# Kernel tuning notes

Hardware: AMD Instinct MI355X
Metric: run time of the kernel (lower is better)

Reference implementation:

```python
import jax, jax.numpy as jnp
import numpy as np

T, B, DIM = 1024, 32, 1024
H, N = 8, 64
INIT_BETA_BIAS = 2.0
EPS = 1e-6


def setup_inputs() -> dict:
    key = jax.random.key(0)
    ks = jax.random.split(key, 5)
    scale = 1.0 / np.sqrt(DIM)  # xavier-ish
    return {
        "x": jax.random.normal(ks[0], (T, B, DIM), dtype=jnp.float32),
        "W_k": jax.random.normal(ks[1], (H * N, DIM), dtype=jnp.float32) * scale,
        "W_v": jax.random.normal(ks[2], (H * N, DIM), dtype=jnp.float32) * scale,
        "W_q": jax.random.normal(ks[3], (H * N, DIM), dtype=jnp.float32) * scale,
        "W_beta": jax.random.normal(ks[4], (H * N, DIM), dtype=jnp.float32) * scale,
        "b_beta": jnp.full((H, N), INIT_BETA_BIAS, dtype=jnp.float32),
    }


def reference(x, W_k, W_v, W_q, W_beta, b_beta):
    Tn, Bn, D = x.shape
    Hn, n = b_beta.shape
    xf = x.reshape(Tn * Bn, D)
    k_all = (xf @ W_k.T).reshape(Tn, Bn, Hn, n)
    v_all = (xf @ W_v.T).reshape(Tn, Bn, Hn, n)
    q_all = (xf @ W_q.T).reshape(Tn, Bn, Hn, n)
    beta_all = jax.nn.sigmoid((xf @ W_beta.T).reshape(Tn, Bn, Hn, n) + b_beta)
    k_norm = k_all / (jnp.linalg.norm(k_all, axis=-1, keepdims=True) + EPS)

    def step(S, inp):
        k, v, q, beta = inp  # each [B, H, n]
        retrieved = jnp.einsum('bhij,bhj->bhi', S, k)
        delta = v - retrieved
        outer = jnp.einsum('bhi,bhj->bhij', delta, k)
        S = jnp.tanh(beta[..., None] * S + outer)
        Sq = jnp.einsum('bhij,bhj->bhi', S, q)
        out = Sq * jax.nn.silu(Sq)  # [B, H, n]
        return S, out.reshape(Bn, Hn * n)

    S0 = jnp.zeros((Bn, Hn, n, n), dtype=x.dtype)
    S_final, output = jax.lax.scan(step, S0, (k_norm, v_all, q_all, beta_all))
    return output, S_final  # output: [T, B, H*n]
```

## Files before the change

### kernel.cpp

```cpp
#include <hip/hip_runtime.h>
#include <stdint.h>

#define TSTEPS 1024
#define BATCH  32
#define DIMK   1024
#define HEADS  8
#define NHEAD  64
#define NPROJ  2048
#define MROWS  (TSTEPS*BATCH)

typedef _Float16 f16;
typedef _Float16 f16x2 __attribute__((ext_vector_type(2)));
typedef _Float16 f16x4 __attribute__((ext_vector_type(4)));
typedef _Float16 f16x8 __attribute__((ext_vector_type(8)));
typedef float    f32x2 __attribute__((ext_vector_type(2)));
typedef float    f32x4 __attribute__((ext_vector_type(4)));
typedef unsigned int u32;

#define AS_GLOBAL __attribute__((address_space(1)))
#define AS_LDS    __attribute__((address_space(3)))

#define C2LOG2E 2.8853900817779268f

__device__ __forceinline__ void load_lds_16B(const void* g, void* l){
  __builtin_amdgcn_global_load_lds((const AS_GLOBAL u32*)g, (AS_LDS u32*)l, 16, 0, 0);
}

__device__ __forceinline__ float sigmoid_fast(float x){
  return __builtin_amdgcn_rcpf(1.0f + __expf(-x));
}

__device__ __forceinline__ float exp2_fast(float x){
#if __has_builtin(__builtin_amdgcn_exp2f)
  return __builtin_amdgcn_exp2f(x);
#else
  return __expf(0.6931471805599453f * x);
#endif
}

__device__ __forceinline__ float fdot2(f16x2 a, f16x2 b, float c){
#if __has_builtin(__builtin_amdgcn_fdot2)
  typedef __fp16 h16x2 __attribute__((ext_vector_type(2)));
  return __builtin_amdgcn_fdot2(__builtin_bit_cast(h16x2, a),
                                __builtin_bit_cast(h16x2, b), c, false);
#else
  return fmaf((float)a[1], (float)b[1], fmaf((float)a[0], (float)b[0], c));
#endif
}

__device__ __forceinline__ f16x2 pack2(float a, float b){
#if __has_builtin(__builtin_amdgcn_cvt_pkrtz)
  return __builtin_bit_cast(f16x2, __builtin_amdgcn_cvt_pkrtz(a, b));
#else
  f16x2 r = { (f16)a, (f16)b };
  return r;
#endif
}

template<int CTRL>
__device__ __forceinline__ float dpp_add(float r){
  int x = __builtin_amdgcn_update_dpp(__builtin_bit_cast(int, r),
                                      __builtin_bit_cast(int, r),
                                      CTRL, 0xf, 0xf, false);
  return r + __builtin_bit_cast(float, x);
}
__device__ __forceinline__ float dpp_reduce16(float r){
  r = dpp_add<0x121>(r);
  r = dpp_add<0x122>(r);
  r = dpp_add<0x124>(r);
  r = dpp_add<0x128>(r);
  return r;
}

__global__ __launch_bounds__(256) void cast_kernel(const float4* __restrict__ src,
                                                   f16x4* __restrict__ dst, int n4){
  int i = blockIdx.x*blockDim.x + threadIdx.x;
  int stride = gridDim.x*blockDim.x;
  for (; i < n4; i += stride){
    float4 v = src[i];
    f16x4 o = { (f16)v.x, (f16)v.y, (f16)v.z, (f16)v.w };
    dst[i] = o;
  }
}

#define BM 128
#define BN 128
#define BK 32

__global__ __launch_bounds__(256) void gemm_xwT(const f16* __restrict__ A,
                                                const f16* __restrict__ B,
                                                f16* __restrict__ C){
  __shared__ f16 sA[BM*BK];
  __shared__ f16 sB[BN*BK];
  const int t = threadIdx.x;
  const int w = t >> 6;
  const int l = t & 63;
  const int bm = blockIdx.x;
  const int bn = blockIdx.y;
  const int wr = w >> 1, wc = w & 1;

  f32x4 acc[4][4] = {};

  const int srow = t >> 2;
  const int scol = (t & 3) * 8;
  const f16* gA0 = A + (size_t)(bm*BM + srow)*DIMK + scol;
  const f16* gB0 = B + (size_t)(bn*BN + srow)*DIMK + scol;
  char* sAb = (char*)sA;
  char* sBb = (char*)sB;
  const int ldsw = w*1024;

  for (int kk = 0; kk < DIMK/BK; ++kk){
    const f16* pa = gA0 + kk*BK;
    const f16* pb = gB0 + kk*BK;
    load_lds_16B(pa,           sAb + ldsw);
    load_lds_16B(pa + 64*DIMK, sAb + ldsw + 4096);
    load_lds_16B(pb,           sBb + ldsw);
    load_lds_16B(pb + 64*DIMK, sBb + ldsw + 4096);
    __syncthreads();

    f16x8 af[4], bf[4];
    #pragma unroll
    for (int mi=0; mi<4; ++mi){
      int arow = wr*64 + mi*16 + (l & 15);
      af[mi] = *(const f16x8*)(sAb + arow*64 + (l>>4)*16);
    }
    #pragma unroll
    for (int ni=0; ni<4; ++ni){
      int brow = wc*64 + ni*16 + (l & 15);
      bf[ni] = *(const f16x8*)(sBb + brow*64 + (l>>4)*16);
    }
    #pragma unroll
    for (int mi=0; mi<4; ++mi)
      #pragma unroll
      for (int ni=0; ni<4; ++ni)
        acc[mi][ni] = __builtin_amdgcn_mfma_f32_16x16x32_f16(af[mi], bf[ni], acc[mi][ni], 0, 0, 0);
    __syncthreads();
  }

  const int crow0 = bm*BM + wr*64 + (l>>4)*4;
  const int ccol0 = bn*BN + wc*64 + (l & 15);
  #pragma unroll
  for (int mi=0; mi<4; ++mi)
    #pragma unroll
    for (int ni=0; ni<4; ++ni)
      #pragma unroll
      for (int r=0; r<4; ++r)
        C[(size_t)(crow0 + mi*16 + r)*NPROJ + ccol0 + ni*16] = (f16)acc[mi][ni][r];
}

__global__ __launch_bounds__(256) void prep_kernel(f16* __restrict__ Y,
                                                   const float* __restrict__ b_beta){
  int g = blockIdx.x*4 + (threadIdx.x >> 6);
  int l = threadIdx.x & 63;
  int h = g & 7;
  f16* y = Y + (size_t)(g >> 3)*NPROJ + h*NHEAD + l;
  float k  = (float)y[0];
  float br = (float)y[1536];
  float ss = k*k;
  #pragma unroll
  for (int d=1; d<64; d<<=1) ss += __shfl_xor(ss, d);
  y[0]    = (f16)(k * __builtin_amdgcn_rcpf(__builtin_sqrtf(ss) + 1e-6f));
  y[1536] = (f16)(C2LOG2E * sigmoid_fast(br + b_beta[h*NHEAD + l]));
}

struct Stage { f16x2 kl, kh, ql, qh; float v, bb; };

__device__ __forceinline__ Stage load_stage(const f16* base, int tn, int cb, int row){
  const f16* pn = base + (size_t)tn * (BATCH*NPROJ);
  Stage s;
  uint2 ku = *(const uint2*)(pn + cb);
  uint2 qu = *(const uint2*)(pn + 1024 + cb);
  s.kl = __builtin_bit_cast(f16x2, ku.x);
  s.kh = __builtin_bit_cast(f16x2, ku.y);
  s.ql = __builtin_bit_cast(f16x2, qu.x);
  s.qh = __builtin_bit_cast(f16x2, qu.y);
  s.v  = (float)pn[512 + row];
  s.bb = (float)pn[1536 + row];
  return s;
}

__device__ __forceinline__ void step_compute(const Stage& st, int tt, int g,
                                             f32x2& S01, f32x2& S23,
                                             f16x2& P0, f16x2& P1,
                                             float* outp){
  float r = fdot2(P1, st.kh, fdot2(P0, st.kl, 0.f));
  r = dpp_reduce16(r);
  float dl = (st.v - r) * C2LOG2E;

  f32x2 d2  = { dl, dl };
  f32x2 bb2 = { st.bb, st.bb };
  f32x2 k01 = { (float)st.kl[0], (float)st.kl[1] };
  f32x2 k23 = { (float)st.kh[0], (float)st.kh[1] };
  f32x2 arg01 = bb2*S01 + d2*k01;
  f32x2 arg23 = bb2*S23 + d2*k23;

  f32x2 e01 = { exp2_fast(arg01.x), exp2_fast(arg01.y) };
  f32x2 e23 = { exp2_fast(arg23.x), exp2_fast(arg23.y) };
  f32x2 one2 = { 1.f, 1.f };
  e01 += one2;  e23 += one2;
  f32x2 t01 = { __builtin_amdgcn_rcpf(e01.x), __builtin_amdgcn_rcpf(e01.y) };
  f32x2 t23 = { __builtin_amdgcn_rcpf(e23.x), __builtin_amdgcn_rcpf(e23.y) };
  f32x2 m2 = { -2.f, -2.f };
  S01 = m2*t01 + one2;
  S23 = m2*t23 + one2;
  P0 = pack2(S01.x, S01.y);
  P1 = pack2(S23.x, S23.y);

  float sq = fdot2(P1, st.qh, fdot2(P0, st.ql, 0.f));
  sq = dpp_reduce16(sq);
  if (g == 0) outp[(size_t)tt * (BATCH*512)] = sq;
}

__global__ __launch_bounds__(1024) void scan_kernel(const f16* __restrict__ Y,
                                                    float* __restrict__ out,
                                                    float* __restrict__ S_out){
  const int p = blockIdx.x;
  const int b = p >> 3, h = p & 7;
  const int t = threadIdx.x;
  const int row = t >> 4;
  const int g   = t & 15;
  const int cb  = g*4;

  f32x2 S01 = {0.f, 0.f}, S23 = {0.f, 0.f};
  f16x2 P0 = {}, P1 = {};

  const f16* base = Y + (size_t)b*NPROJ + h*NHEAD;
  float* outp = out + (size_t)b*512 + h*NHEAD + row;

  Stage s0 = load_stage(base, 0, cb, row);
  Stage s1 = load_stage(base, 1, cb, row);
  Stage s2 = load_stage(base, 2, cb, row);
  Stage s3 = load_stage(base, 3, cb, row);

  #pragma unroll 1
  for (int tt=0; tt<TSTEPS; tt+=4){
    Stage n0 = load_stage(base, tt+4, cb, row);
    step_compute(s0, tt,   g, S01,S23, P0,P1, outp);
    Stage n1 = load_stage(base, tt+5, cb, row);
    step_compute(s1, tt+1, g, S01,S23, P0,P1, outp);
    Stage n2 = load_stage(base, tt+6, cb, row);
    step_compute(s2, tt+2, g, S01,S23, P0,P1, outp);
    Stage n3 = load_stage(base, tt+7, cb, row);
    step_compute(s3, tt+3, g, S01,S23, P0,P1, outp);
    s0 = n0; s1 = n1; s2 = n2; s3 = n3;
  }

  size_t sbase = ((size_t)p*NHEAD + row)*NHEAD + cb;
  float4 v4 = { S01.x, S01.y, S23.x, S23.y };
  *(float4*)(S_out + sbase) = v4;
}

__global__ __launch_bounds__(256) void silu_kernel(float4* __restrict__ o, int n4){
  int i = blockIdx.x*blockDim.x + threadIdx.x;
  int stride = gridDim.x*blockDim.x;
  for (; i < n4; i += stride){
    float4 v = o[i];
    v.x = v.x*v.x*sigmoid_fast(v.x);
    v.y = v.y*v.y*sigmoid_fast(v.y);
    v.z = v.z*v.z*sigmoid_fast(v.z);
    v.w = v.w*v.w*sigmoid_fast(v.w);
    o[i] = v;
  }
}

extern "C" void kernel_launch(void* const* d_in, const int* in_sizes, int n_in,
                              void* d_out, int out_size, void* d_ws, size_t ws_size,
                              hipStream_t stream){
  const float* x  = (const float*)d_in[0];
  const float* Wk = (const float*)d_in[1];
  const float* Wv = (const float*)d_in[2];
  const float* Wq = (const float*)d_in[3];
  const float* Wb = (const float*)d_in[4];
  const float* bb = (const float*)d_in[5];

  float* out = (float*)d_out;
  float* Sf  = out + (size_t)TSTEPS*BATCH*512;

  char* ws = (char*)d_ws;
  f16* Yh = (f16*)ws;
  f16* xh = (f16*)(ws + 134217728);
  f16* wh = (f16*)(ws + 134217728 + 67108864);

  cast_kernel<<<2048, 256, 0, stream>>>((const float4*)x,  (f16x4*)xh, (MROWS*DIMK)/4);
  cast_kernel<<<512,  256, 0, stream>>>((const float4*)Wk, (f16x4*)(wh + 0*524288), 524288/4);
  cast_kernel<<<512,  256, 0, stream>>>((const float4*)Wv, (f16x4*)(wh + 1*524288), 524288/4);
  cast_kernel<<<512,  256, 0, stream>>>((const float4*)Wq, (f16x4*)(wh + 2*524288), 524288/4);
  cast_kernel<<<512,  256, 0, stream>>>((const float4*)Wb, (f16x4*)(wh + 3*524288), 524288/4);

  dim3 g(MROWS/BM, NPROJ/BN);
  gemm_xwT<<<g, 256, 0, stream>>>(xh, wh, Yh);

  prep_kernel<<<(TSTEPS*BATCH*HEADS)/4, 256, 0, stream>>>(Yh, bb);

  scan_kernel<<<256, 1024, 0, stream>>>(Yh, out, Sf);

  silu_kernel<<<2048, 256, 0, stream>>>((float4*)out, (TSTEPS*BATCH*512)/4);
}
```

Measured before the change: 802.5 us.

## Store projections per (batch,head) contiguously and stream scan inputs via LDS double buffer

The GEMM epilogue now writes its output in a [b,h,t,256] layout, with k, q and interleaved v/beta per step, in place of row-major [t*b, 2048]. Each scan block can then read its whole time series contiguously. The scan kernel copies 64-step chunks into a double-buffered LDS region with async global-to-LDS loads, replacing per-step scattered global loads, and the prep kernel is adapted to the new layout. The aim is to take global load latency off the serial recurrence. The cost is scattered 2-byte stores in the GEMM epilogue and a block-wide barrier every 64 steps.

```diff
diff --git a/kernel.cpp b/kernel.cpp
--- a/kernel.cpp
+++ b/kernel.cpp
@@ -89,7 +89,7 @@
 
 __global__ __launch_bounds__(256) void gemm_xwT(const f16* __restrict__ A,
                                                 const f16* __restrict__ B,
-                                                f16* __restrict__ C){
+                                                f16* __restrict__ Zo){
   __shared__ f16 sA[BM*BK];
   __shared__ f16 sB[BN*BK];
   const int t = threadIdx.x;
@@ -140,112 +140,124 @@
   const int crow0 = bm*BM + wr*64 + (l>>4)*4;
   const int ccol0 = bn*BN + wc*64 + (l & 15);
   #pragma unroll
-  for (int mi=0; mi<4; ++mi)
+  for (int ni=0; ni<4; ++ni){
+    int n = ccol0 + ni*16;
+    int stream = n >> 9;
+    int hh = (n >> 6) & 7;
+    int e = n & 63;
+    int eidx = (stream==0) ? e : (stream==2) ? 64+e : (stream==1) ? 128+2*e : 129+2*e;
     #pragma unroll
-    for (int ni=0; ni<4; ++ni)
+    for (int mi=0; mi<4; ++mi)
       #pragma unroll
-      for (int r=0; r<4; ++r)
-        C[(size_t)(crow0 + mi*16 + r)*NPROJ + ccol0 + ni*16] = (f16)acc[mi][ni][r];
-}
-
-__global__ __launch_bounds__(256) void prep_kernel(f16* __restrict__ Y,
+      for (int r=0; r<4; ++r){
+        int m = crow0 + mi*16 + r;
+        int ti = m >> 5, bi = m & 31;
+        size_t zi = ((size_t)(bi*8 + hh)*1024 + ti)*256 + eidx;
+        Zo[zi] = (f16)acc[mi][ni][r];
+      }
+  }
+}
+
+__global__ __launch_bounds__(256) void prep_kernel(f16* __restrict__ Z,
                                                    const float* __restrict__ b_beta){
-  int g = blockIdx.x*4 + (threadIdx.x >> 6);
+  int wid = blockIdx.x*4 + (threadIdx.x >> 6);
   int l = threadIdx.x & 63;
-  int h = g & 7;
-  f16* y = Y + (size_t)(g >> 3)*NPROJ + h*NHEAD + l;
-  float k  = (float)y[0];
-  float br = (float)y[1536];
+  int h = (wid >> 10) & 7;
+  f16* z = Z + (size_t)wid * 256;
+  float k  = (float)z[l];
+  float br = (float)z[129 + 2*l];
   float ss = k*k;
   #pragma unroll
   for (int d=1; d<64; d<<=1) ss += __shfl_xor(ss, d);
-  y[0]    = (f16)(k * __builtin_amdgcn_rcpf(__builtin_sqrtf(ss) + 1e-6f));
-  y[1536] = (f16)(C2LOG2E * sigmoid_fast(br + b_beta[h*NHEAD + l]));
-}
-
-struct Stage { f16x2 kl, kh, ql, qh; float v, bb; };
-
-__device__ __forceinline__ Stage load_stage(const f16* base, int tn, int cb, int row){
-  const f16* pn = base + (size_t)tn * (BATCH*NPROJ);
-  Stage s;
-  uint2 ku = *(const uint2*)(pn + cb);
-  uint2 qu = *(const uint2*)(pn + 1024 + cb);
-  s.kl = __builtin_bit_cast(f16x2, ku.x);
-  s.kh = __builtin_bit_cast(f16x2, ku.y);
-  s.ql = __builtin_bit_cast(f16x2, qu.x);
-  s.qh = __builtin_bit_cast(f16x2, qu.y);
-  s.v  = (float)pn[512 + row];
-  s.bb = (float)pn[1536 + row];
-  return s;
-}
-
-__device__ __forceinline__ void step_compute(const Stage& st, int tt, int g,
-                                             f32x2& S01, f32x2& S23,
-                                             f16x2& P0, f16x2& P1,
-                                             float* outp){
-  float r = fdot2(P1, st.kh, fdot2(P0, st.kl, 0.f));
-  r = dpp_reduce16(r);
-  float dl = (st.v - r) * C2LOG2E;
-
-  f32x2 d2  = { dl, dl };
-  f32x2 bb2 = { st.bb, st.bb };
-  f32x2 k01 = { (float)st.kl[0], (float)st.kl[1] };
-  f32x2 k23 = { (float)st.kh[0], (float)st.kh[1] };
-  f32x2 arg01 = bb2*S01 + d2*k01;
-  f32x2 arg23 = bb2*S23 + d2*k23;
-
-  f32x2 e01 = { exp2_fast(arg01.x), exp2_fast(arg01.y) };
-  f32x2 e23 = { exp2_fast(arg23.x), exp2_fast(arg23.y) };
-  f32x2 one2 = { 1.f, 1.f };
-  e01 += one2;  e23 += one2;
-  f32x2 t01 = { __builtin_amdgcn_rcpf(e01.x), __builtin_amdgcn_rcpf(e01.y) };
-  f32x2 t23 = { __builtin_amdgcn_rcpf(e23.x), __builtin_amdgcn_rcpf(e23.y) };
-  f32x2 m2 = { -2.f, -2.f };
-  S01 = m2*t01 + one2;
-  S23 = m2*t23 + one2;
-  P0 = pack2(S01.x, S01.y);
-  P1 = pack2(S23.x, S23.y);
-
-  float sq = fdot2(P1, st.qh, fdot2(P0, st.ql, 0.f));
-  sq = dpp_reduce16(sq);
-  if (g == 0) outp[(size_t)tt * (BATCH*512)] = sq;
-}
-
-__global__ __launch_bounds__(1024) void scan_kernel(const f16* __restrict__ Y,
+  z[l]       = (f16)(k * __builtin_amdgcn_rcpf(__builtin_sqrtf(ss) + 1e-6f));
+  z[129+2*l] = (f16)(C2LOG2E * sigmoid_fast(br + b_beta[h*NHEAD + l]));
+}
+
+#define STAGE_STEPS 64
+#define STAGE_F16   (STAGE_STEPS*256)
+
+__global__ __launch_bounds__(1024) void scan_kernel(const f16* __restrict__ Z,
                                                     float* __restrict__ out,
                                                     float* __restrict__ S_out){
   const int p = blockIdx.x;
   const int b = p >> 3, h = p & 7;
   const int t = threadIdx.x;
+  const int w = t >> 6;
+  const int lane = t & 63;
   const int row = t >> 4;
   const int g   = t & 15;
-  const int cb  = g*4;
-
-  f32x2 S01 = {0.f, 0.f}, S23 = {0.f, 0.f};
+
+  __shared__ f16 lds[2*STAGE_F16];
+
+  f32x2 S01 = {0.f,0.f}, S23 = {0.f,0.f};
   f16x2 P0 = {}, P1 = {};
 
-  const f16* base = Y + (size_t)b*NPROJ + h*NHEAD;
+  const char* Zp = (const char*)(Z + (size_t)p * (TSTEPS*256));
   float* outp = out + (size_t)b*512 + h*NHEAD + row;
-
-  Stage s0 = load_stage(base, 0, cb, row);
-  Stage s1 = load_stage(base, 1, cb, row);
-  Stage s2 = load_stage(base, 2, cb, row);
-  Stage s3 = load_stage(base, 3, cb, row);
+  char* ldsb = (char*)lds;
+
+  {
+    const char* src = Zp + w*2048 + lane*16;
+    load_lds_16B(src,        ldsb + w*2048);
+    load_lds_16B(src + 1024, ldsb + w*2048 + 1024);
+  }
+  __syncthreads();
 
   #pragma unroll 1
-  for (int tt=0; tt<TSTEPS; tt+=4){
-    Stage n0 = load_stage(base, tt+4, cb, row);
-    step_compute(s0, tt,   g, S01,S23, P0,P1, outp);
-    Stage n1 = load_stage(base, tt+5, cb, row);
-    step_compute(s1, tt+1, g, S01,S23, P0,P1, outp);
-    Stage n2 = load_stage(base, tt+6, cb, row);
-    step_compute(s2, tt+2, g, S01,S23, P0,P1, outp);
-    Stage n3 = load_stage(base, tt+7, cb, row);
-    step_compute(s3, tt+3, g, S01,S23, P0,P1, outp);
-    s0 = n0; s1 = n1; s2 = n2; s3 = n3;
-  }
-
-  size_t sbase = ((size_t)p*NHEAD + row)*NHEAD + cb;
+  for (int st=0; st<TSTEPS/STAGE_STEPS; ++st){
+    if (st < TSTEPS/STAGE_STEPS - 1){
+      const char* src = Zp + (st+1)*(STAGE_F16*2) + w*2048 + lane*16;
+      char* dst = ldsb + ((st+1)&1)*(STAGE_F16*2) + w*2048;
+      load_lds_16B(src,        dst);
+      load_lds_16B(src + 1024, dst + 1024);
+    }
+
+    const f16* buf = lds + (st&1)*STAGE_F16;
+    #pragma unroll 4
+    for (int s=0; s<STAGE_STEPS; ++s){
+      const f16* ps = buf + s*256;
+      f16x4 k4 = *(const f16x4*)(ps + g*4);
+      f16x4 q4 = *(const f16x4*)(ps + 64 + g*4);
+      f16x2 vb = *(const f16x2*)(ps + 128 + row*2);
+
+      uint2 ku = __builtin_bit_cast(uint2, k4);
+      uint2 qu = __builtin_bit_cast(uint2, q4);
+      f16x2 kl = __builtin_bit_cast(f16x2, ku.x), kh = __builtin_bit_cast(f16x2, ku.y);
+      f16x2 ql = __builtin_bit_cast(f16x2, qu.x), qh = __builtin_bit_cast(f16x2, qu.y);
+      float v  = (float)vb[0];
+      float bb = (float)vb[1];
+
+      float r = fdot2(P1, kh, fdot2(P0, kl, 0.f));
+      r = dpp_reduce16(r);
+      float dl = (v - r) * C2LOG2E;
+
+      f32x2 d2  = { dl, dl };
+      f32x2 bb2 = { bb, bb };
+      f32x2 k01 = { (float)kl[0], (float)kl[1] };
+      f32x2 k23 = { (float)kh[0], (float)kh[1] };
+      f32x2 arg01 = bb2*S01 + d2*k01;
+      f32x2 arg23 = bb2*S23 + d2*k23;
+
+      f32x2 e01 = { exp2_fast(arg01.x), exp2_fast(arg01.y) };
+      f32x2 e23 = { exp2_fast(arg23.x), exp2_fast(arg23.y) };
+      f32x2 one2 = { 1.f, 1.f };
+      e01 += one2;  e23 += one2;
+      f32x2 t01 = { __builtin_amdgcn_rcpf(e01.x), __builtin_amdgcn_rcpf(e01.y) };
+      f32x2 t23 = { __builtin_amdgcn_rcpf(e23.x), __builtin_amdgcn_rcpf(e23.y) };
+      f32x2 m2 = { -2.f, -2.f };
+      S01 = m2*t01 + one2;
+      S23 = m2*t23 + one2;
+      P0 = pack2(S01.x, S01.y);
+      P1 = pack2(S23.x, S23.y);
+
+      float sq = fdot2(P1, qh, fdot2(P0, ql, 0.f));
+      sq = dpp_reduce16(sq);
+      if (g == 0) outp[(size_t)(st*STAGE_STEPS + s) * (BATCH*512)] = sq;
+    }
+    __syncthreads();
+  }
+
+  size_t sbase = ((size_t)p*NHEAD + row)*NHEAD + g*4;
   float4 v4 = { S01.x, S01.y, S23.x, S23.y };
   *(float4*)(S_out + sbase) = v4;
 }
@@ -277,7 +289,7 @@
   float* Sf  = out + (size_t)TSTEPS*BATCH*512;
 
   char* ws = (char*)d_ws;
-  f16* Yh = (f16*)ws;
+  f16* Zh = (f16*)ws;
   f16* xh = (f16*)(ws + 134217728);
   f16* wh = (f16*)(ws + 134217728 + 67108864);
 
@@ -288,11 +300,11 @@
   cast_kernel<<<512,  256, 0, stream>>>((const float4*)Wb, (f16x4*)(wh + 3*524288), 524288/4);
 
   dim3 g(MROWS/BM, NPROJ/BN);
-  gemm_xwT<<<g, 256, 0, stream>>>(xh, wh, Yh);
-
-  prep_kernel<<<(TSTEPS*BATCH*HEADS)/4, 256, 0, stream>>>(Yh, bb);
-
-  scan_kernel<<<256, 1024, 0, stream>>>(Yh, out, Sf);
+  gemm_xwT<<<g, 256, 0, stream>>>(xh, wh, Zh);
+
+  prep_kernel<<<(TSTEPS*BATCH*HEADS)/4, 256, 0, stream>>>(Zh, bb);
+
+  scan_kernel<<<256, 1024, 0, stream>>>(Zh, out, Sf);
 
   silu_kernel<<<2048, 256, 0, stream>>>((float4*)out, (TSTEPS*BATCH*512)/4);
 }
```

Result: slower. 840.9 us (+4.8%).
